# Performance work log

Hardware: AMD Instinct MI355X
Metric: run time of the kernel (lower is better)

## Reference

```python
import jax, jax.numpy as jnp
import numpy as np


def _gated_mlp(h, lW1, lb1, lW2, lb2, lW3, lb3, gW1, gb1, gW2, gb2, gW3, gb3):
    # main branch: Linear+SiLU, Linear+SiLU, Linear (activate_last=False)
    m = jax.nn.silu(h @ lW1 + lb1)
    m = jax.nn.silu(m @ lW2 + lb2)
    m = m @ lW3 + lb3
    # gate branch: Linear+SiLU, Linear+SiLU, Linear+Sigmoid
    g = jax.nn.silu(h @ gW1 + gb1)
    g = jax.nn.silu(g @ gW2 + gb2)
    g = jax.nn.sigmoid(g @ gW3 + gb3)
    return m * g


def setup_inputs() -> dict:
    key = jax.random.key(0)
    ks = jax.random.split(key, 7)
    N, F, T = 1024, 64, 1
    s = 1.0 / np.sqrt(F)
    return {
        "node_feat": jax.random.normal(ks[0], (N, F), dtype=jnp.float32),
        "lW1": jax.random.normal(ks[1], (F, F), dtype=jnp.float32) * s,
        "lb1": jnp.zeros((F,), dtype=jnp.float32),
        "lW2": jax.random.normal(ks[2], (F, F), dtype=jnp.float32) * s,
        "lb2": jnp.zeros((F,), dtype=jnp.float32),
        "lW3": jax.random.normal(ks[3], (F, T), dtype=jnp.float32) * s,
        "lb3": jnp.zeros((T,), dtype=jnp.float32),
        "gW1": jax.random.normal(ks[4], (F, F), dtype=jnp.float32) * s,
        "gb1": jnp.zeros((F,), dtype=jnp.float32),
        "gW2": jax.random.normal(ks[5], (F, F), dtype=jnp.float32) * s,
        "gb2": jnp.zeros((F,), dtype=jnp.float32),
        "gW3": jax.random.normal(ks[6], (F, T), dtype=jnp.float32) * s,
        "gb3": jnp.zeros((T,), dtype=jnp.float32),
    }


def reference(node_feat, lW1, lb1, lW2, lb2, lW3, lb3, gW1, gb1, gW2, gb2, gW3, gb3):
    # pairwise average of node features: [N, N, F] (symmetric by construction)
    pair = (node_feat[:, None, :] + node_feat[None, :, :]) * 0.5
    # batched gated MLP over all pairs -> [N, N, num_targets]
    return _gated_mlp(pair, lW1, lb1, lW2, lb2, lW3, lb3, gW1, gb1, gW2, gb2, gW3, gb3)
```

## Files before the change

kernel.cpp:

```cpp
#include <hip/hip_runtime.h>
#include <hip/hip_bf16.h>
#include <math.h>

#define F 64
#define TILE 16

typedef __attribute__((ext_vector_type(8))) short bf16x8;
typedef __attribute__((ext_vector_type(4))) float f32x4;

union BF8 { bf16x8 v; unsigned u[4]; };

#define LOG2E 1.4426950408889634f

__device__ __forceinline__ float fast_exp(float x) {
    return __builtin_amdgcn_exp2f(x * LOG2E);
}
__device__ __forceinline__ float fast_sigmoid(float x) {
    return __builtin_amdgcn_rcpf(1.0f + fast_exp(-x));
}
__device__ __forceinline__ float fast_silu(float x) {
    return x * __builtin_amdgcn_rcpf(1.0f + fast_exp(-x));
}
__device__ __forceinline__ unsigned cvtpk(float a, float b) {
    unsigned r;
    asm("v_cvt_pk_bf16_f32 %0, %1, %2" : "=v"(r) : "v"(a), "v"(b));
    return r;
}
__device__ __forceinline__ short f2bf(float x) {
    __hip_bfloat16 h = __float2bfloat16(x);
    return __builtin_bit_cast(short, h);
}

__global__ void precompute_yz(const float* __restrict__ x,
                              const float* __restrict__ lW1, const float* __restrict__ lb1,
                              const float* __restrict__ gW1, const float* __restrict__ gb1,
                              float* __restrict__ y, float* __restrict__ z) {
    __shared__ float xs[F];
    const int i = blockIdx.x;
    const int f = threadIdx.x;
    xs[f] = x[i * F + f];
    __syncthreads();
    float accY = 0.f, accZ = 0.f;
#pragma unroll
    for (int k = 0; k < F; ++k) {
        const float xv = xs[k];
        accY += xv * lW1[k * F + f];
        accZ += xv * gW1[k * F + f];
    }
    y[i * F + f] = 0.5f * accY + 0.5f * lb1[f];
    z[i * F + f] = 0.5f * accZ + 0.5f * gb1[f];
}

__global__ void prep_wfrags(const float* __restrict__ lW2,
                            const float* __restrict__ gW2,
                            short* __restrict__ wf) {
    const int idx = blockIdx.x * 256 + threadIdx.x;
    const int e    = idx & 7;
    const int lane = (idx >> 3) & 63;
    const int ft   = (idx >> 9) & 3;
    const int kt   = (idx >> 11) & 1;
    const int b    = (idx >> 12) & 1;
    const int k = kt * 32 + ((lane >> 4) << 3) + e;
    const int f = ft * 16 + (lane & 15);
    const float* W = b ? gW2 : lW2;
    wf[idx] = f2bf(W[k * F + f]);
}

__device__ __forceinline__ void run_branch(
    const float (*si)[F + 4], const float (*sj)[F + 4],
    const short* __restrict__ wfb,
    const float* sB2, const float* sW3,
    int w, int g, int c, float (&part)[4]) {

    const int l = g * 16 + c;

    BF8 bf[2][4];
#pragma unroll
    for (int kt = 0; kt < 2; ++kt) {
        const float* pj = &sj[c][kt * 32 + 8 * g];
        const float4 j0v = *(const float4*)(pj);
        const float4 j1v = *(const float4*)(pj + 4);
#pragma unroll
        for (int pt = 0; pt < 4; ++pt) {
            const float* pi = &si[4 * w + pt][kt * 32 + 8 * g];
            const float4 i0v = *(const float4*)(pi);
            const float4 i1v = *(const float4*)(pi + 4);
            bf[kt][pt].u[0] = cvtpk(fast_silu(i0v.x + j0v.x), fast_silu(i0v.y + j0v.y));
            bf[kt][pt].u[1] = cvtpk(fast_silu(i0v.z + j0v.z), fast_silu(i0v.w + j0v.w));
            bf[kt][pt].u[2] = cvtpk(fast_silu(i1v.x + j1v.x), fast_silu(i1v.y + j1v.y));
            bf[kt][pt].u[3] = cvtpk(fast_silu(i1v.z + j1v.z), fast_silu(i1v.w + j1v.w));
        }
    }

    part[0] = part[1] = part[2] = part[3] = 0.f;

#pragma unroll
    for (int ft = 0; ft < 4; ++ft) {
        const short* base = wfb + ft * 512 + l * 8;
        const bf16x8 wh0 = *(const bf16x8*)(base);
        const bf16x8 wh1 = *(const bf16x8*)(base + 2048);
        const float4 b2v = *(const float4*)&sB2[ft * 16 + 4 * g];
        const float4 w3v = *(const float4*)&sW3[ft * 16 + 4 * g];
#pragma unroll
        for (int pt = 0; pt < 4; ++pt) {
            f32x4 acc = (f32x4){b2v.x, b2v.y, b2v.z, b2v.w};
            acc = __builtin_amdgcn_mfma_f32_16x16x32_bf16(wh0, bf[0][pt].v, acc, 0, 0, 0);
            acc = __builtin_amdgcn_mfma_f32_16x16x32_bf16(wh1, bf[1][pt].v, acc, 0, 0, 0);
            part[pt] += fast_silu(acc[0]) * w3v.x
                      + fast_silu(acc[1]) * w3v.y
                      + fast_silu(acc[2]) * w3v.z
                      + fast_silu(acc[3]) * w3v.w;
        }
    }
}

__global__ __launch_bounds__(256) void pair_mlp_mfma(
    const float* __restrict__ y, const float* __restrict__ z,
    const short* __restrict__ wf,
    const float* __restrict__ lb2, const float* __restrict__ lW3, const float* __restrict__ lb3,
    const float* __restrict__ gb2, const float* __restrict__ gW3, const float* __restrict__ gb3,
    float* __restrict__ out, int N) {

    __shared__ __align__(16) float smem[4608];
    float (*ysi)[F + 4] = (float (*)[F + 4])(smem + 0);
    float (*zsi)[F + 4] = (float (*)[F + 4])(smem + 1088);
    float (*ysj)[F + 4] = (float (*)[F + 4])(smem + 2176);
    float (*zsj)[F + 4] = (float (*)[F + 4])(smem + 3264);
    float* sB2l = smem + 4352;
    float* sW3l = smem + 4416;
    float* sB2g = smem + 4480;
    float* sW3g = smem + 4544;
    float (*valD)[TILE + 1] = (float (*)[TILE + 1])(smem + 0);
    float (*valT)[TILE + 1] = (float (*)[TILE + 1])(smem + 1088);

    const int bid = blockIdx.x;
    int tj = (int)((sqrtf(8.0f * (float)bid + 1.0f) - 1.0f) * 0.5f);
    while ((tj + 1) * (tj + 2) / 2 <= bid) ++tj;
    while (tj * (tj + 1) / 2 > bid) --tj;
    const int ti = bid - tj * (tj + 1) / 2;
    const int i0 = ti * TILE, j0 = tj * TILE;

    const int t = threadIdx.x;

    {
        const int r = t >> 4;
        const int e4 = t & 15;
        const float4* yv = (const float4*)y;
        const float4* zv = (const float4*)z;
        *(float4*)&ysi[r][e4 * 4] = yv[(size_t)(i0 + r) * (F / 4) + e4];
        *(float4*)&zsi[r][e4 * 4] = zv[(size_t)(i0 + r) * (F / 4) + e4];
        *(float4*)&ysj[r][e4 * 4] = yv[(size_t)(j0 + r) * (F / 4) + e4];
        *(float4*)&zsj[r][e4 * 4] = zv[(size_t)(j0 + r) * (F / 4) + e4];
    }
    if (t < F) {
        sB2l[t] = lb2[t];
        sW3l[t] = lW3[t];
        sB2g[t] = gb2[t];
        sW3g[t] = gW3[t];
    }
    __syncthreads();

    const int w = t >> 6;
    const int l = t & 63;
    const int g = l >> 4;
    const int c = l & 15;

    float partL[4], partG[4];
    run_branch(ysi, ysj, wf,        sB2l, sW3l, w, g, c, partL);
    run_branch(zsi, zsj, wf + 4096, sB2g, sW3g, w, g, c, partG);

#pragma unroll
    for (int pt = 0; pt < 4; ++pt) {
        partL[pt] += __shfl_xor(partL[pt], 16, 64);
        partL[pt] += __shfl_xor(partL[pt], 32, 64);
        partG[pt] += __shfl_xor(partG[pt], 16, 64);
        partG[pt] += __shfl_xor(partG[pt], 32, 64);
    }

    const float b3l = lb3[0];
    const float b3g = gb3[0];

    __syncthreads();

    if (g == 0) {
#pragma unroll
        for (int pt = 0; pt < 4; ++pt) {
            const float m3 = partL[pt] + b3l;
            const float g3 = partG[pt] + b3g;
            const float v = m3 * fast_sigmoid(g3);
            valD[4 * w + pt][c] = v;
            valT[c][4 * w + pt] = v;
        }
    }
    __syncthreads();

    {
        const int r = t >> 4;
        const int cc = t & 15;
        out[(size_t)(i0 + r) * N + (j0 + cc)] = valD[r][cc];
        out[(size_t)(j0 + r) * N + (i0 + cc)] = valT[r][cc];
    }
}

extern "C" void kernel_launch(void* const* d_in, const int* in_sizes, int n_in,
                              void* d_out, int out_size, void* d_ws, size_t ws_size,
                              hipStream_t stream) {
    const float* node_feat = (const float*)d_in[0];
    const float* lW1 = (const float*)d_in[1];
    const float* lb1 = (const float*)d_in[2];
    const float* lW2 = (const float*)d_in[3];
    const float* lb2 = (const float*)d_in[4];
    const float* lW3 = (const float*)d_in[5];
    const float* lb3 = (const float*)d_in[6];
    const float* gW1 = (const float*)d_in[7];
    const float* gb1 = (const float*)d_in[8];
    const float* gW2 = (const float*)d_in[9];
    const float* gb2 = (const float*)d_in[10];
    const float* gW3 = (const float*)d_in[11];
    const float* gb3 = (const float*)d_in[12];

    const int N = in_sizes[0] / F;

    float* y = (float*)d_ws;
    float* z = y + (size_t)N * F;
    short* wfrag = (short*)(z + (size_t)N * F);

    precompute_yz<<<N, F, 0, stream>>>(node_feat, lW1, lb1, gW1, gb1, y, z);
    prep_wfrags<<<32, 256, 0, stream>>>(lW2, gW2, wfrag);

    const int nT = N / TILE;
    const int nBlocks = nT * (nT + 1) / 2;
    pair_mlp_mfma<<<nBlocks, 256, 0, stream>>>(y, z, wfrag,
                                               lb2, lW3, lb3,
                                               gb2, gW3, gb3,
                                               (float*)d_out, N);
}
```

Measured before the change: 52.26 us.

## Stage W2 fragments in LDS and restructure branch loop to cut register pressure

The bf16 W2 MFMA fragments (16 KB) are now copied cooperatively into shared memory at block start and read from LDS rather than global memory. The per-branch loop is reordered so each pair-row's activations are built and consumed immediately, instead of holding all eight bf16x8 fragments live at once. A minimum-blocks hint of 4 is added to launch bounds. The aim is lower VGPR use for higher occupancy and less repeated global weight traffic, at the cost of more LDS per block, an extra copy per block, and redundant LDS weight reads for each pair-row.

```diff
diff --git a/kernel.cpp b/kernel.cpp
--- a/kernel.cpp
+++ b/kernel.cpp
@@ -68,60 +68,68 @@
 
 __device__ __forceinline__ void run_branch(
     const float (*si)[F + 4], const float (*sj)[F + 4],
-    const short* __restrict__ wfb,
+    const short* swfb,
     const float* sB2, const float* sW3,
     int w, int g, int c, float (&part)[4]) {
 
     const int l = g * 16 + c;
 
-    BF8 bf[2][4];
-#pragma unroll
-    for (int kt = 0; kt < 2; ++kt) {
-        const float* pj = &sj[c][kt * 32 + 8 * g];
-        const float4 j0v = *(const float4*)(pj);
-        const float4 j1v = *(const float4*)(pj + 4);
-#pragma unroll
-        for (int pt = 0; pt < 4; ++pt) {
-            const float* pi = &si[4 * w + pt][kt * 32 + 8 * g];
+#pragma unroll
+    for (int pt = 0; pt < 4; ++pt) {
+        BF8 bf0, bf1;
+        {
+            const float* pj = &sj[c][8 * g];
+            const float4 j0v = *(const float4*)(pj);
+            const float4 j1v = *(const float4*)(pj + 4);
+            const float* pi = &si[4 * w + pt][8 * g];
             const float4 i0v = *(const float4*)(pi);
             const float4 i1v = *(const float4*)(pi + 4);
-            bf[kt][pt].u[0] = cvtpk(fast_silu(i0v.x + j0v.x), fast_silu(i0v.y + j0v.y));
-            bf[kt][pt].u[1] = cvtpk(fast_silu(i0v.z + j0v.z), fast_silu(i0v.w + j0v.w));
-            bf[kt][pt].u[2] = cvtpk(fast_silu(i1v.x + j1v.x), fast_silu(i1v.y + j1v.y));
-            bf[kt][pt].u[3] = cvtpk(fast_silu(i1v.z + j1v.z), fast_silu(i1v.w + j1v.w));
-        }
-    }
-
-    part[0] = part[1] = part[2] = part[3] = 0.f;
-
-#pragma unroll
-    for (int ft = 0; ft < 4; ++ft) {
-        const short* base = wfb + ft * 512 + l * 8;
-        const bf16x8 wh0 = *(const bf16x8*)(base);
-        const bf16x8 wh1 = *(const bf16x8*)(base + 2048);
-        const float4 b2v = *(const float4*)&sB2[ft * 16 + 4 * g];
-        const float4 w3v = *(const float4*)&sW3[ft * 16 + 4 * g];
-#pragma unroll
-        for (int pt = 0; pt < 4; ++pt) {
+            bf0.u[0] = cvtpk(fast_silu(i0v.x + j0v.x), fast_silu(i0v.y + j0v.y));
+            bf0.u[1] = cvtpk(fast_silu(i0v.z + j0v.z), fast_silu(i0v.w + j0v.w));
+            bf0.u[2] = cvtpk(fast_silu(i1v.x + j1v.x), fast_silu(i1v.y + j1v.y));
+            bf0.u[3] = cvtpk(fast_silu(i1v.z + j1v.z), fast_silu(i1v.w + j1v.w));
+        }
+        {
+            const float* pj = &sj[c][32 + 8 * g];
+            const float4 j0v = *(const float4*)(pj);
+            const float4 j1v = *(const float4*)(pj + 4);
+            const float* pi = &si[4 * w + pt][32 + 8 * g];
+            const float4 i0v = *(const float4*)(pi);
+            const float4 i1v = *(const float4*)(pi + 4);
+            bf1.u[0] = cvtpk(fast_silu(i0v.x + j0v.x), fast_silu(i0v.y + j0v.y));
+            bf1.u[1] = cvtpk(fast_silu(i0v.z + j0v.z), fast_silu(i0v.w + j0v.w));
+            bf1.u[2] = cvtpk(fast_silu(i1v.x + j1v.x), fast_silu(i1v.y + j1v.y));
+            bf1.u[3] = cvtpk(fast_silu(i1v.z + j1v.z), fast_silu(i1v.w + j1v.w));
+        }
+
+        float p = 0.f;
+#pragma unroll
+        for (int ft = 0; ft < 4; ++ft) {
+            const short* base = swfb + ft * 512 + l * 8;
+            const bf16x8 wh0 = *(const bf16x8*)(base);
+            const bf16x8 wh1 = *(const bf16x8*)(base + 2048);
+            const float4 b2v = *(const float4*)&sB2[ft * 16 + 4 * g];
+            const float4 w3v = *(const float4*)&sW3[ft * 16 + 4 * g];
             f32x4 acc = (f32x4){b2v.x, b2v.y, b2v.z, b2v.w};
-            acc = __builtin_amdgcn_mfma_f32_16x16x32_bf16(wh0, bf[0][pt].v, acc, 0, 0, 0);
-            acc = __builtin_amdgcn_mfma_f32_16x16x32_bf16(wh1, bf[1][pt].v, acc, 0, 0, 0);
-            part[pt] += fast_silu(acc[0]) * w3v.x
-                      + fast_silu(acc[1]) * w3v.y
-                      + fast_silu(acc[2]) * w3v.z
-                      + fast_silu(acc[3]) * w3v.w;
-        }
-    }
-}
-
-__global__ __launch_bounds__(256) void pair_mlp_mfma(
+            acc = __builtin_amdgcn_mfma_f32_16x16x32_bf16(wh0, bf0.v, acc, 0, 0, 0);
+            acc = __builtin_amdgcn_mfma_f32_16x16x32_bf16(wh1, bf1.v, acc, 0, 0, 0);
+            p += fast_silu(acc[0]) * w3v.x
+               + fast_silu(acc[1]) * w3v.y
+               + fast_silu(acc[2]) * w3v.z
+               + fast_silu(acc[3]) * w3v.w;
+        }
+        part[pt] = p;
+    }
+}
+
+__global__ __launch_bounds__(256, 4) void pair_mlp_mfma(
     const float* __restrict__ y, const float* __restrict__ z,
     const short* __restrict__ wf,
     const float* __restrict__ lb2, const float* __restrict__ lW3, const float* __restrict__ lb3,
     const float* __restrict__ gb2, const float* __restrict__ gW3, const float* __restrict__ gb3,
     float* __restrict__ out, int N) {
 
-    __shared__ __align__(16) float smem[4608];
+    __shared__ __align__(16) float smem[8704];
     float (*ysi)[F + 4] = (float (*)[F + 4])(smem + 0);
     float (*zsi)[F + 4] = (float (*)[F + 4])(smem + 1088);
     float (*ysj)[F + 4] = (float (*)[F + 4])(smem + 2176);
@@ -130,6 +138,7 @@
     float* sW3l = smem + 4416;
     float* sB2g = smem + 4480;
     float* sW3g = smem + 4544;
+    short* swf  = (short*)(smem + 4608);
     float (*valD)[TILE + 1] = (float (*)[TILE + 1])(smem + 0);
     float (*valT)[TILE + 1] = (float (*)[TILE + 1])(smem + 1088);
 
@@ -152,6 +161,13 @@
         *(float4*)&ysj[r][e4 * 4] = yv[(size_t)(j0 + r) * (F / 4) + e4];
         *(float4*)&zsj[r][e4 * 4] = zv[(size_t)(j0 + r) * (F / 4) + e4];
     }
+    {
+        const float4* src = (const float4*)wf;
+        float4* dst = (float4*)swf;
+#pragma unroll
+        for (int r = 0; r < 4; ++r)
+            dst[t + 256 * r] = src[t + 256 * r];
+    }
     if (t < F) {
         sB2l[t] = lb2[t];
         sW3l[t] = lW3[t];
@@ -166,8 +182,8 @@
     const int c = l & 15;
 
     float partL[4], partG[4];
-    run_branch(ysi, ysj, wf,        sB2l, sW3l, w, g, c, partL);
-    run_branch(zsi, zsj, wf + 4096, sB2g, sW3g, w, g, c, partG);
+    run_branch(ysi, ysj, swf,        sB2l, sW3l, w, g, c, partL);
+    run_branch(zsi, zsj, swf + 4096, sB2g, sW3g, w, g, c, partG);
 
 #pragma unroll
     for (int pt = 0; pt < 4; ++pt) {
```

New measurement: 60.81 us. 16.4% more time.
